# Optimization experiments

Hardware: AMD Instinct MI355X
Metric: run time of the kernel (lower is better)

The kernel has to match this reference:

```python
import jax, jax.numpy as jnp
import numpy as np

B, T, D, H = 4, 2048, 1024, 16
Hd = D // H


def setup_inputs() -> dict:
    key = jax.random.key(0)
    ks = jax.random.split(key, 6)
    s = 1.0 / np.sqrt(D)
    return {
        "x": jax.random.normal(ks[0], (B, T, D), dtype=jnp.float32),
        "mask": jnp.zeros((B, T), dtype=bool),
        "Wq": jax.random.normal(ks[1], (D, D), dtype=jnp.float32) * s,
        "bq": jnp.zeros((D,), dtype=jnp.float32),
        "Wk": jax.random.normal(ks[2], (D, D), dtype=jnp.float32) * s,
        "bk": jnp.zeros((D,), dtype=jnp.float32),
        "Wv": jax.random.normal(ks[3], (D, D), dtype=jnp.float32) * s,
        "bv": jnp.zeros((D,), dtype=jnp.float32),
        "Wo": jax.random.normal(ks[4], (D, D), dtype=jnp.float32) * s,
        "bo": jnp.zeros((D,), dtype=jnp.float32),
    }


def reference(x, mask, Wq, bq, Wk, bk, Wv, bv, Wo, bo):
    b, t, d = x.shape
    # projections -> [B, T, H, Hd]
    Q = (x @ Wq + bq).reshape(b, t, H, Hd)
    K = (x @ Wk + bk).reshape(b, t, H, Hd)
    V = (x @ Wv + bv).reshape(b, t, H, Hd)
    scale = jnp.asarray(Hd, x.dtype) ** -0.5
    # full score matrix [B, H, Tq, Tk] (matches the naive torch impl)
    attn = jnp.einsum("bqhd,bkhd->bhqk", Q, K) * scale
    attn = jnp.where(mask[:, None, None, :], jnp.asarray(-1e9, attn.dtype), attn)
    attn = jax.nn.softmax(attn, axis=-1)
    out = jnp.einsum("bhqk,bkhd->bqhd", attn, V).reshape(b, t, d)
    return out @ Wo + bo
```

## Files before the change

### kernel.cpp

```cpp
#include <hip/hip_runtime.h>

using bf16 = __bf16;
typedef bf16 bf16x4 __attribute__((ext_vector_type(4)));
typedef bf16 bf16x8 __attribute__((ext_vector_type(8)));
typedef float f32x4 __attribute__((ext_vector_type(4)));
typedef float f32x8 __attribute__((ext_vector_type(8)));

#define MFMA16(a, b, c) __builtin_amdgcn_mfma_f32_16x16x32_bf16(a, b, c, 0, 0, 0)

constexpr int Bb = 4, Tt = 2048, Dd = 1024, Hh = 16, Hd = 64;
constexpr int Mrows = Bb * Tt;
constexpr float CEXP = 0.18033688011112042f;

__device__ __forceinline__ void gload_lds16(const bf16* g, bf16* lds_base) {
  __builtin_amdgcn_global_load_lds((const __attribute__((address_space(1))) void*)g,
                                   (__attribute__((address_space(3))) void*)lds_base,
                                   16, 0, 0);
}

__global__ void cast_f32_bf16_kernel(const float* __restrict__ in, bf16* __restrict__ out) {
  size_t i = ((size_t)blockIdx.x * 256 + threadIdx.x) * 8;
  f32x8 v = *(const f32x8*)(in + i);
  *(bf16x8*)(out + i) = __builtin_convertvector(v, bf16x8);
}

__global__ void transpose_cast_w4_kernel(const float* __restrict__ Wq, const float* __restrict__ Wk,
                                         const float* __restrict__ Wv, const float* __restrict__ Wo,
                                         bf16* __restrict__ Wt, bf16* __restrict__ Wot) {
  __shared__ alignas(16) float tile[64][68];
  const int tid = threadIdx.x;
  const int n0 = blockIdx.x * 64, k0 = blockIdx.y * 64, z = blockIdx.z;
  const float* W = (z == 0) ? Wq : (z == 1) ? Wk : (z == 2) ? Wv : Wo;
  bf16* dst = (z == 3) ? Wot : (Wt + (size_t)z * Dd * Dd);
  const float scale = (z == 0) ? CEXP : 1.0f;
#pragma unroll
  for (int it = 0; it < 4; ++it) {
    int chunk = tid + it * 256;
    int kr = chunk >> 4, c4 = chunk & 15;
    f32x4 v = *(const f32x4*)(W + (size_t)(k0 + kr) * Dd + n0 + c4 * 4);
    *(f32x4*)&tile[kr][c4 * 4] = v * scale;
  }
  __syncthreads();
#pragma unroll
  for (int it = 0; it < 2; ++it) {
    int chunk = tid + it * 256;
    int n = chunk & 63, k8 = chunk >> 6;
    bf16x8 o;
#pragma unroll
    for (int j = 0; j < 8; ++j) o[j] = (bf16)tile[k8 * 8 + j][n];
    *(bf16x8*)(dst + (size_t)(n0 + n) * Dd + k0 + k8 * 8) = o;
  }
}

__global__ void pack_bias_kernel(const float* __restrict__ bq, const float* __restrict__ bk,
                                 const float* __restrict__ bv, float* __restrict__ outb) {
  int i = blockIdx.x * 256 + threadIdx.x;
  float v = (i < 1024) ? bq[i] * CEXP : (i < 2048 ? bk[i - 1024] : bv[i - 2048]);
  outb[i] = v;
}

constexpr int QBM = 128, QBN = 256, QBK = 32, QNT = Dd / QBK;

#define VMW(n) asm volatile("s_waitcnt vmcnt(" #n ")" ::: "memory")

__global__ __launch_bounds__(512, 2)
void gemm_qkv_kernel(const bf16* __restrict__ A, const bf16* __restrict__ Bt,
                     const float* __restrict__ bias, bf16* __restrict__ QK,
                     bf16* __restrict__ Vt) {
  constexpr int KD = Dd;
  __shared__ alignas(16) bf16 As[3][QBM * QBK];
  __shared__ alignas(16) bf16 Bs[3][QBN * QBK];
  const int tid = threadIdx.x;
  const int lane = tid & 63, wave = tid >> 6;
  const int col = lane & 15, quad = lane >> 4;
  const int wr = wave >> 2, wc = wave & 3;
  const size_t m0 = (size_t)blockIdx.x * QBM, n0 = (size_t)blockIdx.y * QBN;

  const int u = (lane & 7) ^ (lane >> 3);
  const int srow = 2 * (lane >> 3) + (u >> 2);
  const int scol = (u & 3) * 8;
  const bf16* Abase = A + (m0 + srow) * (size_t)KD + scol;
  const bf16* Bbase = Bt + (n0 + srow) * (size_t)KD + scol;

  const int pswz = (((col & 1) << 2) | quad) ^ (col >> 1);
  const int afb = wr * 2048 + (col >> 1) * 64 + pswz * 8;
  const int bfb = wc * 2048 + (col >> 1) * 64 + pswz * 8;

  f32x4 acc[4][4];
#pragma unroll
  for (int i = 0; i < 4; ++i)
#pragma unroll
    for (int j = 0; j < 4; ++j)
#pragma unroll
      for (int r = 0; r < 4; ++r) acc[i][j][r] = 0.f;

#define QSTAGE(t, sl) do { \
    gload_lds16(Abase + (size_t)(t) * QBK + (size_t)(wave * 16) * KD, &As[sl][wave * 512]); \
    gload_lds16(Bbase + (size_t)(t) * QBK + (size_t)(2 * wave) * 16 * KD, &Bs[sl][(2 * wave) * 512]); \
    gload_lds16(Bbase + (size_t)(t) * QBK + (size_t)(2 * wave + 1) * 16 * KD, &Bs[sl][(2 * wave + 1) * 512]); \
  } while (0)

#define QKV_TILE(cur, DOSTAGE, VM) do { \
    bf16x8 af[4], bfv[4]; \
    _Pragma("unroll") for (int j = 0; j < 4; ++j) bfv[j] = *(const bf16x8*)&Bs[cur][bfb + j * 512]; \
    _Pragma("unroll") for (int i = 0; i < 4; ++i) af[i] = *(const bf16x8*)&As[cur][afb + i * 512]; \
    DOSTAGE; \
    asm volatile("s_waitcnt lgkmcnt(0)" ::: "memory"); \
    __builtin_amdgcn_s_setprio(1); \
    _Pragma("unroll") for (int i = 0; i < 4; ++i) \
      _Pragma("unroll") for (int j = 0; j < 4; ++j) acc[i][j] = MFMA16(af[i], bfv[j], acc[i][j]); \
    __builtin_amdgcn_s_setprio(0); \
    VM; \
    __builtin_amdgcn_s_barrier(); \
  } while (0)

  QSTAGE(0, 0);
  QSTAGE(1, 1);
  VMW(3);
  __builtin_amdgcn_s_barrier();

#pragma unroll 1
  for (int t = 0; t < QNT - 2; t += 3) {
    QKV_TILE(0, QSTAGE(t + 2, 2), VMW(3));
    QKV_TILE(1, QSTAGE(t + 3, 0), VMW(3));
    QKV_TILE(2, QSTAGE(t + 4, 1), VMW(3));
  }
  QKV_TILE(0, (void)0, VMW(0));
  QKV_TILE(1, (void)0, (void)0);

  if (n0 < 2048) {
#pragma unroll
    for (int i = 0; i < 4; ++i)
#pragma unroll
      for (int j = 0; j < 4; ++j) {
        size_t row = m0 + wr * 64 + i * 16 + quad * 4;
        size_t c = n0 + wc * 64 + j * 16 + col;
        float bv = bias[c];
#pragma unroll
        for (int r = 0; r < 4; ++r) QK[(row + r) * 2048 + c] = (bf16)(acc[i][j][r] + bv);
      }
  } else {
#pragma unroll
    for (int i = 0; i < 4; ++i)
#pragma unroll
      for (int j = 0; j < 4; ++j) {
        size_t row = m0 + wr * 64 + i * 16 + quad * 4;
        int c = (int)(n0 + wc * 64 + j * 16 + col);
        float bv = bias[c];
        int dall = c - 2048, hh = dall >> 6, dd = dall & 63;
        int bi = (int)(row >> 11), trow = (int)(row & 2047);
        bf16x4 pk;
#pragma unroll
        for (int r = 0; r < 4; ++r) pk[r] = (bf16)(acc[i][j][r] + bv);
        *(bf16x4*)&Vt[((size_t)(bi * Hh + hh) * Hd + dd) * Tt + trow] = pk;
      }
  }
#undef QKV_TILE
#undef QSTAGE
}

__global__ __launch_bounds__(256)
void gemm_bf16_kernel(const bf16* __restrict__ A, const bf16* __restrict__ Bt,
                      const float* __restrict__ bias, float* __restrict__ C,
                      int M, int N, int K) {
  __shared__ alignas(16) bf16 As[128 * 64];
  __shared__ alignas(16) bf16 Bs[128 * 64];
  const int tid = threadIdx.x;
  const int lane = tid & 63, wave = tid >> 6;
  const int col = lane & 15, quad = lane >> 4;
  const int wr = (wave >> 1) * 64, wc = (wave & 1) * 64;
  const size_t m0 = (size_t)blockIdx.x * 128, n0 = (size_t)blockIdx.y * 128;
  const int srow = lane >> 3, schunk = (lane & 7) * 8;

  f32x4 acc[4][4];
#pragma unroll
  for (int i = 0; i < 4; ++i)
#pragma unroll
    for (int j = 0; j < 4; ++j)
#pragma unroll
      for (int r = 0; r < 4; ++r) acc[i][j][r] = 0.f;

  for (int k0 = 0; k0 < K; k0 += 64) {
#pragma unroll
    for (int it = 0; it < 4; ++it) {
      int rbase = it * 32 + wave * 8;
      gload_lds16(A + (m0 + rbase + srow) * (size_t)K + k0 + schunk, &As[rbase * 64]);
      gload_lds16(Bt + (n0 + rbase + srow) * (size_t)K + k0 + schunk, &Bs[rbase * 64]);
    }
    __syncthreads();
#pragma unroll
    for (int kk = 0; kk < 2; ++kk) {
      bf16x8 af[4], bfr[4];
#pragma unroll
      for (int i = 0; i < 4; ++i) af[i] = *(const bf16x8*)&As[(wr + i * 16 + col) * 64 + kk * 32 + quad * 8];
#pragma unroll
      for (int j = 0; j < 4; ++j) bfr[j] = *(const bf16x8*)&Bs[(wc + j * 16 + col) * 64 + kk * 32 + quad * 8];
#pragma unroll
      for (int i = 0; i < 4; ++i)
#pragma unroll
        for (int j = 0; j < 4; ++j) acc[i][j] = MFMA16(af[i], bfr[j], acc[i][j]);
    }
    __syncthreads();
  }
#pragma unroll
  for (int i = 0; i < 4; ++i)
#pragma unroll
    for (int j = 0; j < 4; ++j) {
      size_t row = m0 + wr + i * 16 + quad * 4;
      size_t c = n0 + wc + j * 16 + col;
      float bv = bias[c];
#pragma unroll
      for (int r = 0; r < 4; ++r) C[(row + r) * (size_t)N + c] = acc[i][j][r] + bv;
    }
}

__global__ __launch_bounds__(256, 2)
void flash_attn_kernel(const bf16* __restrict__ qk, const bf16* __restrict__ vt,
                       const unsigned char* __restrict__ mask, bf16* __restrict__ ao) {
  __shared__ alignas(16) bf16 Ks[2][64 * 64];
  __shared__ alignas(16) bf16 Vs[2][64 * 64];

  const int tid = threadIdx.x;
  const int wave = tid >> 6, lane = tid & 63;
  const int col = lane & 15, quad = lane >> 4;
  const int id = blockIdx.x;
  const int hb = id & 63, qi = id >> 6;
  const int h = hb & 15, b = hb >> 4;
  const int qbase0 = qi * 128 + wave * 32;

  const bf16* Qp = qk + (size_t)(b * Tt) * 2048 + h * Hd;
  const bf16* Kp = Qp + 1024;
  const bf16* Vp = vt + ((size_t)(b * Hh + h) * Hd) * Tt;
  const unsigned char* mp = mask + b * Tt;

  unsigned long long anym;
  {
    const unsigned long long* mq = (const unsigned long long*)mp;
    unsigned long long acc = 0;
#pragma unroll
    for (int j = 0; j < 4; ++j) acc |= mq[lane * 4 + j];
    anym = __ballot(acc != 0ull);
  }

  bf16x8 qf[2][2];
#pragma unroll
  for (int t = 0; t < 2; ++t)
#pragma unroll
    for (int kk = 0; kk < 2; ++kk)
      qf[t][kk] = *(const bf16x8*)(Qp + (size_t)(qbase0 + t * 16 + col) * 2048 + kk * 32 + quad * 8);

  const int u = (lane & 7) ^ (lane >> 3);
  const int g0 = 2 * wave, g1 = 2 * wave + 1;
  const bf16* Ksrc0 = Kp + (size_t)(g0 * 8 + (lane >> 3)) * 2048 + u * 8;
  const bf16* Ksrc1 = Kp + (size_t)(g1 * 8 + (lane >> 3)) * 2048 + u * 8;
  const bf16* Vsrc0 = Vp + (size_t)(g0 * 8 + (lane >> 3)) * 2048 + u * 8;
  const bf16* Vsrc1 = Vp + (size_t)(g1 * 8 + (lane >> 3)) * 2048 + u * 8;

  gload_lds16(Ksrc0, &Ks[0][g0 * 512]);
  gload_lds16(Ksrc1, &Ks[0][g1 * 512]);
  gload_lds16(Vsrc0, &Vs[0][g0 * 512]);
  gload_lds16(Vsrc1, &Vs[0][g1 * 512]);
  __syncthreads();

  f32x4 oacc[2][4];
  f32x4 lones[2];
#pragma unroll
  for (int t = 0; t < 2; ++t) {
#pragma unroll
    for (int r = 0; r < 4; ++r) lones[t][r] = 0.f;
#pragma unroll
    for (int n = 0; n < 4; ++n)
#pragma unroll
      for (int r = 0; r < 4; ++r) oacc[t][n][r] = 0.f;
  }
  const f32x4 zero4 = {0.f, 0.f, 0.f, 0.f};
  bf16x8 onev;
#pragma unroll
  for (int j = 0; j < 8; ++j) onev[j] = (bf16)1.0f;

  const int fslot0 = ((0 * 4 + quad) ^ (col & 7)) * 8;
  const int fslot1 = ((1 * 4 + quad) ^ (col & 7)) * 8;
  const int voff = (quad & 1) * 4;

  for (int i = 0; i < 32; ++i) {
    const int cur = i & 1, nxt = cur ^ 1;
    const int kb = i * 64;

    if (i < 31) {
      gload_lds16(Ksrc0 + (size_t)(kb + 64) * 2048, &Ks[nxt][g0 * 512]);
      gload_lds16(Ksrc1 + (size_t)(kb + 64) * 2048, &Ks[nxt][g1 * 512]);
      gload_lds16(Vsrc0 + (kb + 64), &Vs[nxt][g0 * 512]);
      gload_lds16(Vsrc1 + (kb + 64), &Vs[nxt][g1 * 512]);
    }

    bf16x8 kf[4][2], vfs[4][2];
#pragma unroll
    for (int kt = 0; kt < 4; ++kt) {
      kf[kt][0] = *(const bf16x8*)&Ks[cur][(kt * 16 + col) * 64 + fslot0];
      kf[kt][1] = *(const bf16x8*)&Ks[cur][(kt * 16 + col) * 64 + fslot1];
    }
#pragma unroll
    for (int n = 0; n < 4; ++n) {
      const int row = (n * 16 + col) * 64;
      const int rx = col & 7;
#pragma unroll
      for (int kk = 0; kk < 2; ++kk) {
        bf16x4 lo = *(const bf16x4*)&Vs[cur][row + ((kk * 4 + 0 + (quad >> 1)) ^ rx) * 8 + voff];
        bf16x4 hi = *(const bf16x4*)&Vs[cur][row + ((kk * 4 + 2 + (quad >> 1)) ^ rx) * 8 + voff];
        vfs[n][kk] = __builtin_shufflevector(lo, hi, 0, 1, 2, 3, 4, 5, 6, 7);
      }
    }

#pragma unroll
    for (int t = 0; t < 2; ++t) {
      f32x4 s[4];
      __builtin_amdgcn_s_setprio(1);
#pragma unroll
      for (int kt = 0; kt < 4; ++kt) s[kt] = MFMA16(kf[kt][0], qf[t][0], zero4);
#pragma unroll
      for (int kt = 0; kt < 4; ++kt) s[kt] = MFMA16(kf[kt][1], qf[t][1], s[kt]);
      __builtin_amdgcn_s_setprio(0);

      if ((anym >> (2 * i)) & 3ull) {
#pragma unroll
        for (int kt = 0; kt < 4; ++kt)
#pragma unroll
          for (int r = 0; r < 4; ++r)
            if (mp[kb + kt * 16 + quad * 4 + r] != 0) s[kt][r] = -1e9f;
      }

      f32x4 e[4];
#pragma unroll
      for (int kt = 0; kt < 4; ++kt)
#pragma unroll
        for (int r = 0; r < 4; ++r) e[kt][r] = __builtin_amdgcn_exp2f(s[kt][r]);
      bf16x4 c0 = __builtin_convertvector(e[0], bf16x4);
      bf16x4 c1 = __builtin_convertvector(e[1], bf16x4);
      bf16x4 c2 = __builtin_convertvector(e[2], bf16x4);
      bf16x4 c3 = __builtin_convertvector(e[3], bf16x4);
      bf16x8 pf0 = __builtin_shufflevector(c0, c1, 0, 1, 2, 3, 4, 5, 6, 7);
      bf16x8 pf1 = __builtin_shufflevector(c2, c3, 0, 1, 2, 3, 4, 5, 6, 7);
      __builtin_amdgcn_s_setprio(1);
#pragma unroll
      for (int n = 0; n < 4; ++n) {
        oacc[t][n] = MFMA16(pf0, vfs[n][0], oacc[t][n]);
        oacc[t][n] = MFMA16(pf1, vfs[n][1], oacc[t][n]);
      }
      lones[t] = MFMA16(pf0, onev, lones[t]);
      lones[t] = MFMA16(pf1, onev, lones[t]);
      __builtin_amdgcn_s_setprio(0);
    }

    __syncthreads();
  }

#pragma unroll
  for (int t = 0; t < 2; ++t) {
    f32x4 rl;
#pragma unroll
    for (int r = 0; r < 4; ++r) rl[r] = __builtin_amdgcn_rcpf(lones[t][r]);
#pragma unroll
    for (int n = 0; n < 4; ++n)
#pragma unroll
      for (int r = 0; r < 4; ++r) {
        size_t q = (size_t)b * Tt + qbase0 + t * 16 + quad * 4 + r;
        ao[q * Dd + h * Hd + n * 16 + col] = (bf16)(oacc[t][n][r] * rl[r]);
      }
  }
}

extern "C" void kernel_launch(void* const* d_in, const int* in_sizes, int n_in,
                              void* d_out, int out_size, void* d_ws, size_t ws_size,
                              hipStream_t stream) {
  const float* x = (const float*)d_in[0];
  const unsigned char* mask = (const unsigned char*)d_in[1];
  const float* Wq = (const float*)d_in[2];
  const float* bq = (const float*)d_in[3];
  const float* Wk = (const float*)d_in[4];
  const float* bk = (const float*)d_in[5];
  const float* Wv = (const float*)d_in[6];
  const float* bv = (const float*)d_in[7];
  const float* Wo = (const float*)d_in[8];
  const float* bo = (const float*)d_in[9];
  float* out = (float*)d_out;

  char* ws = (char*)d_ws;
  size_t off = 0;
  auto alloc = [&](size_t bytes) {
    char* p = ws + off;
    off += (bytes + 255) & ~(size_t)255;
    return p;
  };
  bf16* xb  = (bf16*)alloc((size_t)Mrows * Dd * 2);
  bf16* Wt  = (bf16*)alloc((size_t)3 * Dd * Dd * 2);
  bf16* Wot = (bf16*)alloc((size_t)Dd * Dd * 2);
  bf16* QK  = (bf16*)alloc((size_t)Mrows * 2048 * 2);
  bf16* Vt  = (bf16*)alloc((size_t)Bb * Hh * Hd * Tt * 2);
  float* bqkv = (float*)alloc((size_t)3 * Dd * 4);

  cast_f32_bf16_kernel<<<Mrows * Dd / (256 * 8), 256, 0, stream>>>(x, xb);
  transpose_cast_w4_kernel<<<dim3(16, 16, 4), 256, 0, stream>>>(Wq, Wk, Wv, Wo, Wt, Wot);
  pack_bias_kernel<<<12, 256, 0, stream>>>(bq, bk, bv, bqkv);

  gemm_qkv_kernel<<<dim3(Mrows / QBM, 3 * Dd / QBN), 512, 0, stream>>>(
      xb, Wt, bqkv, QK, Vt);

  bf16* AO = xb;
  flash_attn_kernel<<<dim3(1024), 256, 0, stream>>>(QK, Vt, mask, AO);
  gemm_bf16_kernel<<<dim3(Mrows / 128, Dd / 128), 256, 0, stream>>>(
      AO, Wot, bo, out, Mrows, Dd, Dd);
}
```

Baseline: 294.3 us.

## Triple-buffer K/V tiles in flash attention with vmcnt waits and raw barriers

Grows the K/V LDS staging from two to three buffers and hand-unrolls the key loop by three, so loads are issued two tiles ahead. Each iteration now waits only on its own tile's global-to-LDS loads via a vmcnt-based wait, then uses a bare s_barrier instead of __syncthreads. It also drops the s_setprio hints around the MFMA groups. The aim is to hide more global-load latency and cut barrier overhead, at the cost of 16 KB more LDS per block and more code size.

```diff
diff --git a/kernel.cpp b/kernel.cpp
--- a/kernel.cpp
+++ b/kernel.cpp
@@ -217,8 +217,8 @@
 __global__ __launch_bounds__(256, 2)
 void flash_attn_kernel(const bf16* __restrict__ qk, const bf16* __restrict__ vt,
                        const unsigned char* __restrict__ mask, bf16* __restrict__ ao) {
-  __shared__ alignas(16) bf16 Ks[2][64 * 64];
-  __shared__ alignas(16) bf16 Vs[2][64 * 64];
+  __shared__ alignas(16) bf16 Ks[3][64 * 64];
+  __shared__ alignas(16) bf16 Vs[3][64 * 64];
 
   const int tid = threadIdx.x;
   const int wave = tid >> 6, lane = tid & 63;
@@ -256,11 +256,12 @@
   const bf16* Vsrc0 = Vp + (size_t)(g0 * 8 + (lane >> 3)) * 2048 + u * 8;
   const bf16* Vsrc1 = Vp + (size_t)(g1 * 8 + (lane >> 3)) * 2048 + u * 8;
 
-  gload_lds16(Ksrc0, &Ks[0][g0 * 512]);
-  gload_lds16(Ksrc1, &Ks[0][g1 * 512]);
-  gload_lds16(Vsrc0, &Vs[0][g0 * 512]);
-  gload_lds16(Vsrc1, &Vs[0][g1 * 512]);
-  __syncthreads();
+#define FSTAGE(t, sl) do { \
+    gload_lds16(Ksrc0 + (size_t)(t) * 64 * 2048, &Ks[sl][g0 * 512]); \
+    gload_lds16(Ksrc1 + (size_t)(t) * 64 * 2048, &Ks[sl][g1 * 512]); \
+    gload_lds16(Vsrc0 + (t) * 64, &Vs[sl][g0 * 512]); \
+    gload_lds16(Vsrc1 + (t) * 64, &Vs[sl][g1 * 512]); \
+  } while (0)
 
   f32x4 oacc[2][4];
   f32x4 lones[2];
@@ -282,77 +283,68 @@
   const int fslot1 = ((1 * 4 + quad) ^ (col & 7)) * 8;
   const int voff = (quad & 1) * 4;
 
-  for (int i = 0; i < 32; ++i) {
-    const int cur = i & 1, nxt = cur ^ 1;
-    const int kb = i * 64;
-
-    if (i < 31) {
-      gload_lds16(Ksrc0 + (size_t)(kb + 64) * 2048, &Ks[nxt][g0 * 512]);
-      gload_lds16(Ksrc1 + (size_t)(kb + 64) * 2048, &Ks[nxt][g1 * 512]);
-      gload_lds16(Vsrc0 + (kb + 64), &Vs[nxt][g0 * 512]);
-      gload_lds16(Vsrc1 + (kb + 64), &Vs[nxt][g1 * 512]);
-    }
-
-    bf16x8 kf[4][2], vfs[4][2];
-#pragma unroll
-    for (int kt = 0; kt < 4; ++kt) {
-      kf[kt][0] = *(const bf16x8*)&Ks[cur][(kt * 16 + col) * 64 + fslot0];
-      kf[kt][1] = *(const bf16x8*)&Ks[cur][(kt * 16 + col) * 64 + fslot1];
-    }
-#pragma unroll
-    for (int n = 0; n < 4; ++n) {
-      const int row = (n * 16 + col) * 64;
-      const int rx = col & 7;
-#pragma unroll
-      for (int kk = 0; kk < 2; ++kk) {
-        bf16x4 lo = *(const bf16x4*)&Vs[cur][row + ((kk * 4 + 0 + (quad >> 1)) ^ rx) * 8 + voff];
-        bf16x4 hi = *(const bf16x4*)&Vs[cur][row + ((kk * 4 + 2 + (quad >> 1)) ^ rx) * 8 + voff];
-        vfs[n][kk] = __builtin_shufflevector(lo, hi, 0, 1, 2, 3, 4, 5, 6, 7);
-      }
-    }
-
-#pragma unroll
-    for (int t = 0; t < 2; ++t) {
-      f32x4 s[4];
-      __builtin_amdgcn_s_setprio(1);
-#pragma unroll
-      for (int kt = 0; kt < 4; ++kt) s[kt] = MFMA16(kf[kt][0], qf[t][0], zero4);
-#pragma unroll
-      for (int kt = 0; kt < 4; ++kt) s[kt] = MFMA16(kf[kt][1], qf[t][1], s[kt]);
-      __builtin_amdgcn_s_setprio(0);
-
-      if ((anym >> (2 * i)) & 3ull) {
-#pragma unroll
-        for (int kt = 0; kt < 4; ++kt)
-#pragma unroll
-          for (int r = 0; r < 4; ++r)
-            if (mp[kb + kt * 16 + quad * 4 + r] != 0) s[kt][r] = -1e9f;
-      }
-
-      f32x4 e[4];
-#pragma unroll
-      for (int kt = 0; kt < 4; ++kt)
-#pragma unroll
-        for (int r = 0; r < 4; ++r) e[kt][r] = __builtin_amdgcn_exp2f(s[kt][r]);
-      bf16x4 c0 = __builtin_convertvector(e[0], bf16x4);
-      bf16x4 c1 = __builtin_convertvector(e[1], bf16x4);
-      bf16x4 c2 = __builtin_convertvector(e[2], bf16x4);
-      bf16x4 c3 = __builtin_convertvector(e[3], bf16x4);
-      bf16x8 pf0 = __builtin_shufflevector(c0, c1, 0, 1, 2, 3, 4, 5, 6, 7);
-      bf16x8 pf1 = __builtin_shufflevector(c2, c3, 0, 1, 2, 3, 4, 5, 6, 7);
-      __builtin_amdgcn_s_setprio(1);
-#pragma unroll
-      for (int n = 0; n < 4; ++n) {
-        oacc[t][n] = MFMA16(pf0, vfs[n][0], oacc[t][n]);
-        oacc[t][n] = MFMA16(pf1, vfs[n][1], oacc[t][n]);
-      }
-      lones[t] = MFMA16(pf0, onev, lones[t]);
-      lones[t] = MFMA16(pf1, onev, lones[t]);
-      __builtin_amdgcn_s_setprio(0);
-    }
-
-    __syncthreads();
-  }
+#define FITER(cur, II, DOSTAGE, VM) do { \
+    const int kb = (II) * 64; \
+    DOSTAGE; \
+    bf16x8 kf[4][2], vfs[4][2]; \
+    _Pragma("unroll") for (int kt = 0; kt < 4; ++kt) { \
+      kf[kt][0] = *(const bf16x8*)&Ks[cur][(kt * 16 + col) * 64 + fslot0]; \
+      kf[kt][1] = *(const bf16x8*)&Ks[cur][(kt * 16 + col) * 64 + fslot1]; \
+    } \
+    _Pragma("unroll") for (int n = 0; n < 4; ++n) { \
+      const int row = (n * 16 + col) * 64; \
+      const int rx = col & 7; \
+      _Pragma("unroll") for (int kk = 0; kk < 2; ++kk) { \
+        bf16x4 lo = *(const bf16x4*)&Vs[cur][row + ((kk * 4 + 0 + (quad >> 1)) ^ rx) * 8 + voff]; \
+        bf16x4 hi = *(const bf16x4*)&Vs[cur][row + ((kk * 4 + 2 + (quad >> 1)) ^ rx) * 8 + voff]; \
+        vfs[n][kk] = __builtin_shufflevector(lo, hi, 0, 1, 2, 3, 4, 5, 6, 7); \
+      } \
+    } \
+    _Pragma("unroll") for (int t = 0; t < 2; ++t) { \
+      f32x4 s[4]; \
+      _Pragma("unroll") for (int kt = 0; kt < 4; ++kt) s[kt] = MFMA16(kf[kt][0], qf[t][0], zero4); \
+      _Pragma("unroll") for (int kt = 0; kt < 4; ++kt) s[kt] = MFMA16(kf[kt][1], qf[t][1], s[kt]); \
+      if ((anym >> (2 * (II))) & 3ull) { \
+        _Pragma("unroll") for (int kt = 0; kt < 4; ++kt) \
+          _Pragma("unroll") for (int r = 0; r < 4; ++r) \
+            if (mp[kb + kt * 16 + quad * 4 + r] != 0) s[kt][r] = -1e9f; \
+      } \
+      f32x4 e[4]; \
+      _Pragma("unroll") for (int kt = 0; kt < 4; ++kt) \
+        _Pragma("unroll") for (int r = 0; r < 4; ++r) e[kt][r] = __builtin_amdgcn_exp2f(s[kt][r]); \
+      bf16x4 c0 = __builtin_convertvector(e[0], bf16x4); \
+      bf16x4 c1 = __builtin_convertvector(e[1], bf16x4); \
+      bf16x4 c2 = __builtin_convertvector(e[2], bf16x4); \
+      bf16x4 c3 = __builtin_convertvector(e[3], bf16x4); \
+      bf16x8 pf0 = __builtin_shufflevector(c0, c1, 0, 1, 2, 3, 4, 5, 6, 7); \
+      bf16x8 pf1 = __builtin_shufflevector(c2, c3, 0, 1, 2, 3, 4, 5, 6, 7); \
+      _Pragma("unroll") for (int n = 0; n < 4; ++n) { \
+        oacc[t][n] = MFMA16(pf0, vfs[n][0], oacc[t][n]); \
+        oacc[t][n] = MFMA16(pf1, vfs[n][1], oacc[t][n]); \
+      } \
+      lones[t] = MFMA16(pf0, onev, lones[t]); \
+      lones[t] = MFMA16(pf1, onev, lones[t]); \
+    } \
+    VM; \
+    __builtin_amdgcn_s_barrier(); \
+  } while (0)
+
+  FSTAGE(0, 0);
+  FSTAGE(1, 1);
+  VMW(4);
+  __builtin_amdgcn_s_barrier();
+
+#pragma unroll 1
+  for (int ii = 0; ii < 30; ii += 3) {
+    FITER(0, ii + 0, FSTAGE(ii + 2, 2), VMW(4));
+    FITER(1, ii + 1, FSTAGE(ii + 3, 0), VMW(4));
+    FITER(2, ii + 2, FSTAGE(ii + 4, 1), VMW(4));
+  }
+  FITER(0, 30, (void)0, VMW(0));
+  FITER(1, 31, (void)0, (void)0);
+
+#undef FITER
+#undef FSTAGE
 
 #pragma unroll
   for (int t = 0; t < 2; ++t) {
```

New measurement: 284.7 us. 1.03x faster.
